# Optimization experiments

Measured on AMD Instinct MI355X. Metric: run time of the kernel, lower is better.

Reference implementation:

```python
import jax, jax.numpy as jnp
import numpy as np

D_MODEL = 1024
N_HEADS = 16
D_HEAD = D_MODEL // N_HEADS
ROPE_BASE = 10000.0
B, L = 2, 2048


def setup_inputs() -> dict:
    key = jax.random.key(0)
    k1, k2, k3 = jax.random.split(key, 3)
    x = jax.random.normal(k1, (B, L, D_MODEL), dtype=jnp.float32)
    W_qkv = jax.random.normal(k2, (3 * D_MODEL, D_MODEL), dtype=jnp.float32) * (1.0 / np.sqrt(D_MODEL))
    W_out = jax.random.normal(k3, (D_MODEL, D_MODEL), dtype=jnp.float32) * (1.0 / np.sqrt(D_MODEL))
    position_ids = jnp.broadcast_to(jnp.arange(L, dtype=jnp.int32), (B, L))
    attn_mask_2d = jnp.broadcast_to(jnp.tril(jnp.ones((L, L), dtype=bool)), (B, L, L))
    return {"x": x, "W_qkv": W_qkv, "W_out": W_out,
            "position_ids": position_ids, "attn_mask_2d": attn_mask_2d}


def _apply_rope(t, position_ids, inv_freq):
    # t: (B, H, L, Dh) float32; position_ids: (B, L) int
    f = position_ids.astype(jnp.float32)[:, :, None] * inv_freq  # (B, L, Dh/2)
    cos = jnp.cos(f)[:, None]  # (B, 1, L, Dh/2)
    sin = jnp.sin(f)[:, None]
    x1 = t[..., 0::2]
    x2 = t[..., 1::2]
    rot_even = x1 * cos - x2 * sin
    rot_odd = x1 * sin + x2 * cos
    return jnp.stack((rot_even, rot_odd), axis=-1).reshape(t.shape)


def reference(x, W_qkv, W_out, position_ids, attn_mask_2d):
    Bb, Ll, D = x.shape
    H, Dh = N_HEADS, D // N_HEADS
    inv_freq = 1.0 / (ROPE_BASE ** (jnp.arange(0, Dh, 2, dtype=jnp.float32) / Dh))  # (Dh/2,)
    qkv = jnp.einsum('bld,ed->ble', x, W_qkv).reshape(Bb, Ll, 3, H, Dh)
    qkv = jnp.transpose(qkv, (2, 0, 3, 1, 4))  # (3, B, H, L, Dh)
    q, k, v = qkv[0], qkv[1], qkv[2]
    q = _apply_rope(q.astype(jnp.float32), position_ids, inv_freq).astype(x.dtype)
    k = _apply_rope(k.astype(jnp.float32), position_ids, inv_freq).astype(x.dtype)
    scale = 1.0 / np.sqrt(Dh).astype(np.float32)
    scores = jnp.einsum('bhld,bhmd->bhlm', q, k) * scale  # (B, H, L, L)
    neg = jnp.finfo(scores.dtype).min
    scores = jnp.where(attn_mask_2d[:, None], scores, neg)
    attn = jax.nn.softmax(scores, axis=-1)
    out = jnp.einsum('bhlm,bhmd->bhld', attn, v)
    out = jnp.transpose(out, (0, 2, 1, 3)).reshape(Bb, Ll, D)
    return jnp.einsum('bld,ed->ble', out, W_out)
```

## Files before the change

kernel.cpp:

```cpp
#include <hip/hip_runtime.h>
#include <hip/hip_bf16.h>
#include <math.h>

typedef float f32x4 __attribute__((ext_vector_type(4)));
typedef __bf16 bf16x8 __attribute__((ext_vector_type(8)));

__device__ inline f32x4 mfma16(bf16x8 a, bf16x8 b, f32x4 c) {
    return __builtin_amdgcn_mfma_f32_16x16x32_bf16(a, b, c, 0, 0, 0);
}
__device__ inline unsigned short f2bf(float f) {
    union { float f; unsigned u; } v; v.f = f;
    unsigned r = v.u + 0x7fffu + ((v.u >> 16) & 1u);
    return (unsigned short)(r >> 16);
}
__device__ inline float bf2f(unsigned short b) {
    union { unsigned u; float f; } v; v.u = ((unsigned)b) << 16;
    return v.f;
}
__device__ inline unsigned pack2(float a, float b) {
    return (unsigned)f2bf(a) | ((unsigned)f2bf(b) << 16);
}
__device__ inline f32x4 vzero() { f32x4 z = {0.f, 0.f, 0.f, 0.f}; return z; }

#define GLD16(gptr, lptr)                                                            \
    __builtin_amdgcn_global_load_lds(                                                \
        (const __attribute__((address_space(1))) unsigned int*)(const void*)(gptr),  \
        (__attribute__((address_space(3))) unsigned int*)(void*)(lptr), 16, 0, 0)

__global__ void detect_dtype(const unsigned* __restrict__ x, int* __restrict__ flag) {
    __shared__ int cnt;
    int t = threadIdx.x;
    if (t == 0) cnt = 0;
    __syncthreads();
    unsigned w = x[(size_t)t * 8000 + 5];
    unsigned e = (w >> 7) & 0xFFu;
    int plausible = (e >= 100u && e <= 140u) ? 1 : 0;
    atomicAdd(&cnt, plausible);
    __syncthreads();
    if (t == 0) flag[0] = (cnt < 128) ? 1 : 0;
}

__global__ __launch_bounds__(256)
void convert_all(const void* __restrict__ x, const void* __restrict__ wqkv,
                 const void* __restrict__ wout,
                 unsigned short* __restrict__ xb, unsigned short* __restrict__ wqkvb,
                 unsigned short* __restrict__ woutb, const int* __restrict__ flagp)
{
    int i = blockIdx.x * 256 + threadIdx.x;
    const void* src; unsigned short* dst; int off;
    if (i < 524288)      { src = x;    dst = xb;    off = i; }
    else if (i < 917504) { src = wqkv; dst = wqkvb; off = i - 524288; }
    else                 { src = wout; dst = woutb; off = i - 917504; }
    if (flagp[0]) {
        const float4* p = (const float4*)src + (size_t)off * 2;
        float4 f0 = p[0], f1 = p[1];
        uint4 o;
        o.x = pack2(f0.x, f0.y); o.y = pack2(f0.z, f0.w);
        o.z = pack2(f1.x, f1.y); o.w = pack2(f1.z, f1.w);
        ((uint4*)dst)[off] = o;
    } else {
        ((uint4*)dst)[off] = ((const uint4*)src)[off];
    }
}

__global__ __launch_bounds__(256, 3)
void gemm_bt(const unsigned short* __restrict__ A,
             const unsigned short* __restrict__ Wt,
             void* __restrict__ C_, int M, int N, int K,
             const int* __restrict__ flagp, int cFlex)
{
    __shared__ __align__(16) unsigned short As[128 * 64];
    __shared__ __align__(16) unsigned short Bs[128 * 64];

    const bool c32 = (cFlex != 0) && (flagp[0] != 0);
    const int tid  = threadIdx.x;
    const int wave = tid >> 6;
    const int lane = tid & 63;
    const int quad = lane >> 4;
    const int c0   = lane & 15;
    const int m0 = blockIdx.y * 128;
    const int n0 = blockIdx.x * 128;
    const int wm = (wave >> 1) * 64;
    const int wn = (wave & 1) * 64;

    const int lrow   = lane >> 3;
    const int gchunk = (lane & 7) ^ lrow;
    const int goff   = gchunk * 8;

    f32x4 acc[4][4];
#pragma unroll
    for (int i = 0; i < 4; i++)
#pragma unroll
        for (int j = 0; j < 4; j++) acc[i][j] = vzero();

    for (int k0 = 0; k0 < K; k0 += 64) {
        __syncthreads();
#pragma unroll
        for (int p = 0; p < 4; p++) {
            int r0 = p * 32 + wave * 8;
            GLD16(&A[(size_t)(m0 + r0 + lrow) * K + k0 + goff], &As[r0 * 64]);
            GLD16(&Wt[(size_t)(n0 + r0 + lrow) * K + k0 + goff], &Bs[r0 * 64]);
        }
        __syncthreads();
#pragma unroll
        for (int kk = 0; kk < 2; kk++) {
            bf16x8 af[4], bfr[4];
#pragma unroll
            for (int i = 0; i < 4; i++) {
                int row = wm + i * 16 + c0;
                int pos = ((kk * 4 + quad) ^ (c0 & 7)) * 8;
                af[i] = *(const bf16x8*)&As[row * 64 + pos];
            }
#pragma unroll
            for (int j = 0; j < 4; j++) {
                int row = wn + j * 16 + c0;
                int pos = ((kk * 4 + quad) ^ (c0 & 7)) * 8;
                bfr[j] = *(const bf16x8*)&Bs[row * 64 + pos];
            }
#pragma unroll
            for (int i = 0; i < 4; i++)
#pragma unroll
                for (int j = 0; j < 4; j++)
                    acc[i][j] = mfma16(af[i], bfr[j], acc[i][j]);
        }
    }

#pragma unroll
    for (int i = 0; i < 4; i++)
#pragma unroll
        for (int j = 0; j < 4; j++)
#pragma unroll
            for (int r = 0; r < 4; r++) {
                int row  = m0 + wm + i * 16 + quad * 4 + r;
                int colg = n0 + wn + j * 16 + c0;
                if (c32) ((float*)C_)[(size_t)row * N + colg] = acc[i][j][r];
                else ((unsigned short*)C_)[(size_t)row * N + colg] = f2bf(acc[i][j][r]);
            }
}

__global__ __launch_bounds__(256)
void rope_vtrans(const unsigned short* __restrict__ qkv,
                 const int* __restrict__ pos,
                 unsigned short* __restrict__ Qb,
                 unsigned short* __restrict__ Kb,
                 unsigned short* __restrict__ Vt)
{
    __shared__ unsigned short T[256 * 64];
    const int id = blockIdx.x;
    if (id < 8192) {
        int tid = id * 256 + threadIdx.x;
        int d2 = tid & 31;
        int h  = (tid >> 5) & 15;
        int l  = (tid >> 9) & 2047;
        int b  = tid >> 20;
        size_t row = (size_t)(b * 2048 + l) * 3072;
        int col = h * 64 + 2 * d2;
        float inv_freq = exp2f((float)(-2 * d2) * (13.287712379549449f / 64.0f));
        float f = (float)pos[b * 2048 + l] * inv_freq;
        float s, c;
        sincosf(f, &s, &c);
        unsigned qw = *(const unsigned*)&qkv[row + col];
        unsigned kw = *(const unsigned*)&qkv[row + 1024 + col];
        float q1 = bf2f((unsigned short)qw), q2 = bf2f((unsigned short)(qw >> 16));
        float k1 = bf2f((unsigned short)kw), k2 = bf2f((unsigned short)(kw >> 16));
        const float qs = 0.18033688011112042f;
        size_t o = ((size_t)((b * 16 + h) * 2048 + l)) * 64 + 2 * d2;
        *(unsigned*)&Qb[o] = pack2((q1 * c - q2 * s) * qs, (q1 * s + q2 * c) * qs);
        *(unsigned*)&Kb[o] = pack2(k1 * c - k2 * s, k1 * s + k2 * c);
    } else {
        const int id2 = id - 8192;
        const int t = threadIdx.x;
        const int l0 = (id2 & 7) * 256, h = (id2 >> 3) & 15, b = id2 >> 7;
#pragma unroll
        for (int i = 0; i < 8; i++) {
            int c = t + i * 256;
            int r = c >> 3, c8 = c & 7;
            int p = (c8 + (r >> 3)) & 7;
            *(uint4*)&T[r * 64 + p * 8] =
                *(const uint4*)&qkv[(size_t)(b * 2048 + l0 + r) * 3072 + 2048 + h * 64 + c8 * 8];
        }
        __syncthreads();
#pragma unroll
        for (int i = 0; i < 8; i++) {
            int c = t + i * 256;
            int dh = c >> 5, lc = c & 31;
            int blk = dh >> 3;
            unsigned short tmp[8];
#pragma unroll
            for (int j = 0; j < 8; j++) {
                int l = lc * 8 + j;
                int p = (blk + lc) & 7;
                tmp[j] = T[l * 64 + p * 8 + (dh & 7)];
            }
            *(uint4*)&Vt[((size_t)(b * 16 + h) * 64 + dh) * 2048 + l0 + lc * 8] = *(uint4*)tmp;
        }
    }
}

__global__ __launch_bounds__(256, 4)
void attn(const unsigned short* __restrict__ Q,
          const unsigned short* __restrict__ Kb,
          const unsigned short* __restrict__ Vt,
          unsigned short* __restrict__ O)
{
    __shared__ unsigned short Qs[64 * 72];
    __shared__ unsigned short Ks[64 * 72];
    __shared__ unsigned short Vts[64 * 72];
    __shared__ unsigned short Ps[64 * 64];

    const int tid  = threadIdx.x;
    const int wave = tid >> 6;
    const int lane = tid & 63;
    const int quad = lane >> 4;
    const int c0   = lane & 15;
    const int id = blockIdx.x;
    const int qt = 31 - (id >> 5);
    const int h  = id & 15;
    const int b  = (id >> 4) & 1;
    const size_t headoff = ((size_t)(b * 16 + h)) * 2048 * 64;
    const int q0 = qt * 64;
    const float C = 11.541560327111707f;

    const int ca = tid, cb = tid + 256;
    const int ra = ca >> 3, c8a = ca & 7;
    const int rb = cb >> 3, c8b = cb & 7;

    bf16x8 ones;
#pragma unroll
    for (int j = 0; j < 8; j++) ones[j] = (__bf16)1.0f;

    uint4 kreg0, kreg1, vreg0, vreg1;
    {
        kreg0 = *(const uint4*)&Kb[headoff + (size_t)ra * 64 + c8a * 8];
        kreg1 = *(const uint4*)&Kb[headoff + (size_t)rb * 64 + c8b * 8];
        vreg0 = *(const uint4*)&Vt[headoff + (size_t)ra * 2048 + c8a * 8];
        vreg1 = *(const uint4*)&Vt[headoff + (size_t)rb * 2048 + c8b * 8];
    }
#pragma unroll
    for (int i = 0; i < 2; i++) {
        int c = tid + i * 256;
        int r = c >> 3, c8 = c & 7;
        *(uint4*)&Qs[r * 72 + c8 * 8] =
            *(const uint4*)&Q[headoff + (size_t)(q0 + r) * 64 + c8 * 8];
    }

    f32x4 o[4];
#pragma unroll
    for (int j = 0; j < 4; j++) o[j] = vzero();
    f32x4 lacc = vzero();

    for (int kt = 0; kt <= qt; kt++) {
        __syncthreads();
        *(uint4*)&Ks[ra * 72 + c8a * 8] = kreg0;
        *(uint4*)&Ks[rb * 72 + c8b * 8] = kreg1;
        *(uint4*)&Vts[ra * 72 + c8a * 8] = vreg0;
        *(uint4*)&Vts[rb * 72 + c8b * 8] = vreg1;
        __syncthreads();
        if (kt < qt) {
            size_t k1o = headoff + (size_t)(kt + 1) * 4096;
            kreg0 = *(const uint4*)&Kb[k1o + (size_t)ra * 64 + c8a * 8];
            kreg1 = *(const uint4*)&Kb[k1o + (size_t)rb * 64 + c8b * 8];
            vreg0 = *(const uint4*)&Vt[headoff + (size_t)ra * 2048 + (kt + 1) * 64 + c8a * 8];
            vreg1 = *(const uint4*)&Vt[headoff + (size_t)rb * 2048 + (kt + 1) * 64 + c8b * 8];
        }

        f32x4 s[4];
#pragma unroll
        for (int nj = 0; nj < 4; nj++) s[nj] = vzero();
#pragma unroll
        for (int kk = 0; kk < 2; kk++) {
            const int col = kk * 32 + quad * 8;
            bf16x8 aq = *(const bf16x8*)&Qs[(wave * 16 + c0) * 72 + col];
#pragma unroll
            for (int nj = 0; nj < 4; nj++) {
                bf16x8 bk = *(const bf16x8*)&Ks[(nj * 16 + c0) * 72 + col];
                s[nj] = mfma16(aq, bk, s[nj]);
            }
        }
        if (kt == qt) {
#pragma unroll
            for (int nj = 0; nj < 4; nj++)
#pragma unroll
                for (int r = 0; r < 4; r++) {
                    int key  = nj * 16 + c0;
                    int qrow = wave * 16 + quad * 4 + r;
                    if (key > qrow) s[nj][r] = -1e38f;
                }
        }
#pragma unroll
        for (int nj = 0; nj < 4; nj++)
#pragma unroll
            for (int r = 0; r < 4; r++) {
                float p = __builtin_amdgcn_exp2f(s[nj][r] - C);
                int row = wave * 16 + quad * 4 + r;
                int col = nj * 16 + c0;
                int pp = ((col >> 3) + row) & 7;
                Ps[row * 64 + pp * 8 + (col & 7)] = f2bf(p);
            }
        __syncthreads();
#pragma unroll
        for (int kk = 0; kk < 2; kk++) {
            const int col = kk * 32 + quad * 8;
            int prow = wave * 16 + c0;
            int pp = ((kk * 4 + quad) + prow) & 7;
            bf16x8 ap = *(const bf16x8*)&Ps[prow * 64 + pp * 8];
            lacc = mfma16(ap, ones, lacc);
#pragma unroll
            for (int cj = 0; cj < 4; cj++) {
                bf16x8 bv = *(const bf16x8*)&Vts[(cj * 16 + c0) * 72 + col];
                o[cj] = mfma16(ap, bv, o[cj]);
            }
        }
    }

#pragma unroll
    for (int r = 0; r < 4; r++) {
        float inv = 1.0f / lacc[r];
        int ql = q0 + wave * 16 + quad * 4 + r;
        size_t base = ((size_t)b * 2048 + ql) * 1024 + h * 64;
#pragma unroll
        for (int cj = 0; cj < 4; cj++)
            O[base + cj * 16 + c0] = f2bf(o[cj][r] * inv);
    }
}

extern "C" void kernel_launch(void* const* d_in, const int* in_sizes, int n_in,
                              void* d_out, int out_size, void* d_ws, size_t ws_size,
                              hipStream_t stream) {
    const int* pos = (const int*)d_in[3];

    int* flag = (int*)d_ws;
    unsigned short* regA = (unsigned short*)d_ws + 8;
    unsigned short* regB = regA + (size_t)4096 * 1024;
    unsigned short* regC = regB + (size_t)4096 * 1024;
    unsigned short* regD = regC + (size_t)4096 * 1024;
    unsigned short* regE = regD + (size_t)4096 * 3072;

    unsigned short* xb    = regA;
    unsigned short* wqkvb = regB;
    unsigned short* qkv   = regD;
    unsigned short* Qb    = regA;
    unsigned short* Kb    = regB;
    unsigned short* Vt    = regC;
    unsigned short* Ob    = regD;
    unsigned short* woutb = regE;

    detect_dtype<<<1, 256, 0, stream>>>((const unsigned*)d_in[0], flag);
    convert_all<<<4096, 256, 0, stream>>>(d_in[0], d_in[1], d_in[2], xb, wqkvb, woutb, flag);
    gemm_bt<<<dim3(24, 32), 256, 0, stream>>>(xb, wqkvb, qkv, 4096, 3072, 1024, flag, 0);
    rope_vtrans<<<8448, 256, 0, stream>>>(qkv, pos, Qb, Kb, Vt);
    attn<<<1024, 256, 0, stream>>>(Qb, Kb, Vt, Ob);
    gemm_bt<<<dim3(8, 32), 256, 0, stream>>>(Ob, woutb, d_out, 4096, 1024, 1024, flag, 1);
}
```

Before: 235.5 us.

## Drop dtype detection, template GEMM tile, swizzle attention LDS, truncate P

Removes the runtime dtype-detection kernel and flag, assuming float32 inputs. The GEMM is templated on M-tile height and output type, and the output projection uses a 64-row tile to launch more blocks. The attention kernel replaces padded 72-stride LDS tiles with XOR-swizzled 64-stride tiles, which shrinks shared memory and raises the occupancy hint to 5. It also converts P to bf16 by truncation instead of round-to-nearest, trading a little precision for fewer instructions.

```diff
diff --git a/kernel.cpp b/kernel.cpp
--- a/kernel.cpp
+++ b/kernel.cpp
@@ -27,98 +27,79 @@
         (const __attribute__((address_space(1))) unsigned int*)(const void*)(gptr),  \
         (__attribute__((address_space(3))) unsigned int*)(void*)(lptr), 16, 0, 0)
 
-__global__ void detect_dtype(const unsigned* __restrict__ x, int* __restrict__ flag) {
-    __shared__ int cnt;
-    int t = threadIdx.x;
-    if (t == 0) cnt = 0;
-    __syncthreads();
-    unsigned w = x[(size_t)t * 8000 + 5];
-    unsigned e = (w >> 7) & 0xFFu;
-    int plausible = (e >= 100u && e <= 140u) ? 1 : 0;
-    atomicAdd(&cnt, plausible);
-    __syncthreads();
-    if (t == 0) flag[0] = (cnt < 128) ? 1 : 0;
-}
-
 __global__ __launch_bounds__(256)
-void convert_all(const void* __restrict__ x, const void* __restrict__ wqkv,
-                 const void* __restrict__ wout,
+void convert_all(const float* __restrict__ x, const float* __restrict__ wqkv,
+                 const float* __restrict__ wout,
                  unsigned short* __restrict__ xb, unsigned short* __restrict__ wqkvb,
-                 unsigned short* __restrict__ woutb, const int* __restrict__ flagp)
+                 unsigned short* __restrict__ woutb)
 {
     int i = blockIdx.x * 256 + threadIdx.x;
-    const void* src; unsigned short* dst; int off;
+    const float* src; unsigned short* dst; int off;
     if (i < 524288)      { src = x;    dst = xb;    off = i; }
     else if (i < 917504) { src = wqkv; dst = wqkvb; off = i - 524288; }
     else                 { src = wout; dst = woutb; off = i - 917504; }
-    if (flagp[0]) {
-        const float4* p = (const float4*)src + (size_t)off * 2;
-        float4 f0 = p[0], f1 = p[1];
-        uint4 o;
-        o.x = pack2(f0.x, f0.y); o.y = pack2(f0.z, f0.w);
-        o.z = pack2(f1.x, f1.y); o.w = pack2(f1.z, f1.w);
-        ((uint4*)dst)[off] = o;
-    } else {
-        ((uint4*)dst)[off] = ((const uint4*)src)[off];
-    }
-}
-
+    const float4* p = (const float4*)src + (size_t)off * 2;
+    float4 f0 = p[0], f1 = p[1];
+    uint4 o;
+    o.x = pack2(f0.x, f0.y); o.y = pack2(f0.z, f0.w);
+    o.z = pack2(f1.x, f1.y); o.w = pack2(f1.z, f1.w);
+    ((uint4*)dst)[off] = o;
+}
+
+template<int MI, int C32>
 __global__ __launch_bounds__(256, 3)
 void gemm_bt(const unsigned short* __restrict__ A,
              const unsigned short* __restrict__ Wt,
-             void* __restrict__ C_, int M, int N, int K,
-             const int* __restrict__ flagp, int cFlex)
+             void* __restrict__ C_, int M, int N, int K)
 {
-    __shared__ __align__(16) unsigned short As[128 * 64];
+    __shared__ __align__(16) unsigned short As[MI * 32 * 64];
     __shared__ __align__(16) unsigned short Bs[128 * 64];
 
-    const bool c32 = (cFlex != 0) && (flagp[0] != 0);
     const int tid  = threadIdx.x;
     const int wave = tid >> 6;
     const int lane = tid & 63;
     const int quad = lane >> 4;
     const int c0   = lane & 15;
-    const int m0 = blockIdx.y * 128;
+    const int m0 = blockIdx.y * (MI * 32);
     const int n0 = blockIdx.x * 128;
-    const int wm = (wave >> 1) * 64;
+    const int wm = (wave >> 1) * (MI * 16);
     const int wn = (wave & 1) * 64;
 
     const int lrow   = lane >> 3;
     const int gchunk = (lane & 7) ^ lrow;
     const int goff   = gchunk * 8;
 
-    f32x4 acc[4][4];
-#pragma unroll
-    for (int i = 0; i < 4; i++)
+    f32x4 acc[MI][4];
+#pragma unroll
+    for (int i = 0; i < MI; i++)
 #pragma unroll
         for (int j = 0; j < 4; j++) acc[i][j] = vzero();
 
     for (int k0 = 0; k0 < K; k0 += 64) {
         __syncthreads();
+#pragma unroll
+        for (int p = 0; p < MI; p++) {
+            int r0 = p * 32 + wave * 8;
+            GLD16(&A[(size_t)(m0 + r0 + lrow) * K + k0 + goff], &As[r0 * 64]);
+        }
 #pragma unroll
         for (int p = 0; p < 4; p++) {
             int r0 = p * 32 + wave * 8;
-            GLD16(&A[(size_t)(m0 + r0 + lrow) * K + k0 + goff], &As[r0 * 64]);
             GLD16(&Wt[(size_t)(n0 + r0 + lrow) * K + k0 + goff], &Bs[r0 * 64]);
         }
         __syncthreads();
 #pragma unroll
         for (int kk = 0; kk < 2; kk++) {
-            bf16x8 af[4], bfr[4];
-#pragma unroll
-            for (int i = 0; i < 4; i++) {
-                int row = wm + i * 16 + c0;
-                int pos = ((kk * 4 + quad) ^ (c0 & 7)) * 8;
-                af[i] = *(const bf16x8*)&As[row * 64 + pos];
-            }
-#pragma unroll
-            for (int j = 0; j < 4; j++) {
-                int row = wn + j * 16 + c0;
-                int pos = ((kk * 4 + quad) ^ (c0 & 7)) * 8;
-                bfr[j] = *(const bf16x8*)&Bs[row * 64 + pos];
-            }
-#pragma unroll
-            for (int i = 0; i < 4; i++)
+            const int pos = ((kk * 4 + quad) ^ (c0 & 7)) * 8;
+            bf16x8 af[MI], bfr[4];
+#pragma unroll
+            for (int i = 0; i < MI; i++)
+                af[i] = *(const bf16x8*)&As[(wm + i * 16 + c0) * 64 + pos];
+#pragma unroll
+            for (int j = 0; j < 4; j++)
+                bfr[j] = *(const bf16x8*)&Bs[(wn + j * 16 + c0) * 64 + pos];
+#pragma unroll
+            for (int i = 0; i < MI; i++)
 #pragma unroll
                 for (int j = 0; j < 4; j++)
                     acc[i][j] = mfma16(af[i], bfr[j], acc[i][j]);
@@ -126,14 +107,14 @@
     }
 
 #pragma unroll
-    for (int i = 0; i < 4; i++)
+    for (int i = 0; i < MI; i++)
 #pragma unroll
         for (int j = 0; j < 4; j++)
 #pragma unroll
             for (int r = 0; r < 4; r++) {
                 int row  = m0 + wm + i * 16 + quad * 4 + r;
                 int colg = n0 + wn + j * 16 + c0;
-                if (c32) ((float*)C_)[(size_t)row * N + colg] = acc[i][j][r];
+                if (C32) ((float*)C_)[(size_t)row * N + colg] = acc[i][j][r];
                 else ((unsigned short*)C_)[(size_t)row * N + colg] = f2bf(acc[i][j][r]);
             }
 }
@@ -197,15 +178,15 @@
     }
 }
 
-__global__ __launch_bounds__(256, 4)
+__global__ __launch_bounds__(256, 5)
 void attn(const unsigned short* __restrict__ Q,
           const unsigned short* __restrict__ Kb,
           const unsigned short* __restrict__ Vt,
           unsigned short* __restrict__ O)
 {
-    __shared__ unsigned short Qs[64 * 72];
-    __shared__ unsigned short Ks[64 * 72];
-    __shared__ unsigned short Vts[64 * 72];
+    __shared__ unsigned short Qs[64 * 64];
+    __shared__ unsigned short Ks[64 * 64];
+    __shared__ unsigned short Vts[64 * 64];
     __shared__ unsigned short Ps[64 * 64];
 
     const int tid  = threadIdx.x;
@@ -224,6 +205,8 @@
     const int ca = tid, cb = tid + 256;
     const int ra = ca >> 3, c8a = ca & 7;
     const int rb = cb >> 3, c8b = cb & 7;
+    const int la = ra * 64 + (c8a ^ (ra & 7)) * 8;
+    const int lb = rb * 64 + (c8b ^ (rb & 7)) * 8;
 
     bf16x8 ones;
 #pragma unroll
@@ -236,13 +219,8 @@
         vreg0 = *(const uint4*)&Vt[headoff + (size_t)ra * 2048 + c8a * 8];
         vreg1 = *(const uint4*)&Vt[headoff + (size_t)rb * 2048 + c8b * 8];
     }
-#pragma unroll
-    for (int i = 0; i < 2; i++) {
-        int c = tid + i * 256;
-        int r = c >> 3, c8 = c & 7;
-        *(uint4*)&Qs[r * 72 + c8 * 8] =
-            *(const uint4*)&Q[headoff + (size_t)(q0 + r) * 64 + c8 * 8];
-    }
+    *(uint4*)&Qs[la] = *(const uint4*)&Q[headoff + (size_t)(q0 + ra) * 64 + c8a * 8];
+    *(uint4*)&Qs[lb] = *(const uint4*)&Q[headoff + (size_t)(q0 + rb) * 64 + c8b * 8];
 
     f32x4 o[4];
 #pragma unroll
@@ -251,10 +229,10 @@
 
     for (int kt = 0; kt <= qt; kt++) {
         __syncthreads();
-        *(uint4*)&Ks[ra * 72 + c8a * 8] = kreg0;
-        *(uint4*)&Ks[rb * 72 + c8b * 8] = kreg1;
-        *(uint4*)&Vts[ra * 72 + c8a * 8] = vreg0;
-        *(uint4*)&Vts[rb * 72 + c8b * 8] = vreg1;
+        *(uint4*)&Ks[la] = kreg0;
+        *(uint4*)&Ks[lb] = kreg1;
+        *(uint4*)&Vts[la] = vreg0;
+        *(uint4*)&Vts[lb] = vreg1;
         __syncthreads();
         if (kt < qt) {
             size_t k1o = headoff + (size_t)(kt + 1) * 4096;
@@ -269,11 +247,11 @@
         for (int nj = 0; nj < 4; nj++) s[nj] = vzero();
 #pragma unroll
         for (int kk = 0; kk < 2; kk++) {
-            const int col = kk * 32 + quad * 8;
-            bf16x8 aq = *(const bf16x8*)&Qs[(wave * 16 + c0) * 72 + col];
+            const int pos = ((kk * 4 + quad) ^ (c0 & 7)) * 8;
+            bf16x8 aq = *(const bf16x8*)&Qs[(wave * 16 + c0) * 64 + pos];
 #pragma unroll
             for (int nj = 0; nj < 4; nj++) {
-                bf16x8 bk = *(const bf16x8*)&Ks[(nj * 16 + c0) * 72 + col];
+                bf16x8 bk = *(const bf16x8*)&Ks[(nj * 16 + c0) * 64 + pos];
                 s[nj] = mfma16(aq, bk, s[nj]);
             }
         }
@@ -291,23 +269,24 @@
         for (int nj = 0; nj < 4; nj++)
 #pragma unroll
             for (int r = 0; r < 4; r++) {
-                float p = __builtin_amdgcn_exp2f(s[nj][r] - C);
+                union { float f; unsigned u; } pv;
+                pv.f = __builtin_amdgcn_exp2f(s[nj][r] - C);
                 int row = wave * 16 + quad * 4 + r;
                 int col = nj * 16 + c0;
                 int pp = ((col >> 3) + row) & 7;
-                Ps[row * 64 + pp * 8 + (col & 7)] = f2bf(p);
+                Ps[row * 64 + pp * 8 + (col & 7)] = (unsigned short)(pv.u >> 16);
             }
         __syncthreads();
 #pragma unroll
         for (int kk = 0; kk < 2; kk++) {
-            const int col = kk * 32 + quad * 8;
+            const int pos = ((kk * 4 + quad) ^ (c0 & 7)) * 8;
             int prow = wave * 16 + c0;
             int pp = ((kk * 4 + quad) + prow) & 7;
             bf16x8 ap = *(const bf16x8*)&Ps[prow * 64 + pp * 8];
             lacc = mfma16(ap, ones, lacc);
 #pragma unroll
             for (int cj = 0; cj < 4; cj++) {
-                bf16x8 bv = *(const bf16x8*)&Vts[(cj * 16 + c0) * 72 + col];
+                bf16x8 bv = *(const bf16x8*)&Vts[(cj * 16 + c0) * 64 + pos];
                 o[cj] = mfma16(ap, bv, o[cj]);
             }
         }
@@ -329,8 +308,7 @@
                               hipStream_t stream) {
     const int* pos = (const int*)d_in[3];
 
-    int* flag = (int*)d_ws;
-    unsigned short* regA = (unsigned short*)d_ws + 8;
+    unsigned short* regA = (unsigned short*)d_ws;
     unsigned short* regB = regA + (size_t)4096 * 1024;
     unsigned short* regC = regB + (size_t)4096 * 1024;
     unsigned short* regD = regC + (size_t)4096 * 1024;
@@ -345,10 +323,10 @@
     unsigned short* Ob    = regD;
     unsigned short* woutb = regE;
 
-    detect_dtype<<<1, 256, 0, stream>>>((const unsigned*)d_in[0], flag);
-    convert_all<<<4096, 256, 0, stream>>>(d_in[0], d_in[1], d_in[2], xb, wqkvb, woutb, flag);
-    gemm_bt<<<dim3(24, 32), 256, 0, stream>>>(xb, wqkvb, qkv, 4096, 3072, 1024, flag, 0);
+    convert_all<<<4096, 256, 0, stream>>>((const float*)d_in[0], (const float*)d_in[1],
+                                          (const float*)d_in[2], xb, wqkvb, woutb);
+    gemm_bt<4, 0><<<dim3(24, 32), 256, 0, stream>>>(xb, wqkvb, qkv, 4096, 3072, 1024);
     rope_vtrans<<<8448, 256, 0, stream>>>(qkv, pos, Qb, Kb, Vt);
     attn<<<1024, 256, 0, stream>>>(Qb, Kb, Vt, Ob);
-    gemm_bt<<<dim3(8, 32), 256, 0, stream>>>(Ob, woutb, d_out, 4096, 1024, 1024, flag, 1);
-}
+    gemm_bt<2, 1><<<dim3(8, 64), 256, 0, stream>>>(Ob, woutb, d_out, 4096, 1024, 1024);
+}
```

Measured after the change: 213.6 us. -9.3%, faster.
